# Kernel optimization log

Hardware: AMD Instinct MI355X
Metric: run time of the kernel (lower is better)

## Reference

```python
import jax, jax.numpy as jnp
import numpy as np

N_NODES = 100000  # static number of output segments for SpMM


def setup_inputs() -> dict:
    key = jax.random.key(0)
    k_x, k_r, k_c, k_v, k_w, k_b = jax.random.split(key, 6)
    N, E, F_IN, F_OUT = N_NODES, 1600000, 256, 128
    return {
        "input_features": jax.random.normal(k_x, (N, F_IN), dtype=jnp.float32),
        "edge_rows": jax.random.randint(k_r, (E,), 0, N, dtype=jnp.int32),
        "edge_cols": jax.random.randint(k_c, (E,), 0, N, dtype=jnp.int32),
        "edge_vals": jax.random.uniform(k_v, (E,), dtype=jnp.float32),
        "W": jax.random.normal(k_w, (F_OUT, F_IN), dtype=jnp.float32) * 0.02,
        "b": jax.random.normal(k_b, (F_OUT,), dtype=jnp.float32) * 0.02,
    }


def reference(input_features, edge_rows, edge_cols, edge_vals, W, b):
    # transformed = Linear(x) = x @ W^T + b   -> [N, F_OUT]
    transformed = jnp.einsum("nf,of->no", input_features, W) + b
    # SpMM: out[r] = sum_{edges e with row r} val[e] * transformed[col[e]]
    gathered = transformed[edge_cols] * edge_vals[:, None]  # [E, F_OUT]
    out = jax.ops.segment_sum(gathered, edge_rows, num_segments=N_NODES)
    return out
```

## Files before the change

kernel.cpp:

```cpp
#include <hip/hip_runtime.h>

#define N_NODES 100000
#define F_IN 256
#define F_OUT 128
#define NB 1563
#define SUBCAP 256

typedef __attribute__((ext_vector_type(8))) short bf16x8;
typedef __attribute__((ext_vector_type(4))) float f32x4;

__device__ inline unsigned short f2bf(float f) {
  unsigned u = __builtin_bit_cast(unsigned, f);
  u += 0x7fffu + ((u >> 16) & 1u);
  return (unsigned short)(u >> 16);
}

__device__ inline int xcd_id() {
  return __builtin_amdgcn_s_getreg((3 << 11) | (0 << 6) | 20) & 7;
}

__global__ __launch_bounds__(256) void gemm_kernel(
    const float* __restrict__ x, const float* __restrict__ W,
    const float* __restrict__ b, unsigned short* __restrict__ tout) {
  __shared__ unsigned short As[128][72];
  __shared__ unsigned short Bs[128][72];
  const int tid = threadIdx.x;
  const int wave = tid >> 6, lane = tid & 63;
  const int quad = lane >> 4, l16 = lane & 15;
  const int mw = (wave >> 1) * 64, nw = (wave & 1) * 64;
  const int blockM = blockIdx.x * 128;

  f32x4 acc[4][4];
#pragma unroll
  for (int i = 0; i < 4; ++i)
#pragma unroll
    for (int j = 0; j < 4; ++j) acc[i][j] = (f32x4){0.f, 0.f, 0.f, 0.f};

  const int row_s = tid >> 4;
  const int c4 = tid & 15;

  for (int kb = 0; kb < F_IN; kb += 64) {
#pragma unroll
    for (int i = 0; i < 8; ++i) {
      int r = row_s + i * 16;
      int node = blockM + r;
      float4 v = make_float4(0.f, 0.f, 0.f, 0.f);
      if (node < N_NODES) v = *(const float4*)(x + (size_t)node * F_IN + kb + c4 * 4);
      unsigned short* p = &As[r][c4 * 4];
      p[0] = f2bf(v.x); p[1] = f2bf(v.y); p[2] = f2bf(v.z); p[3] = f2bf(v.w);
    }
#pragma unroll
    for (int i = 0; i < 8; ++i) {
      int r = row_s + i * 16;
      float4 v = *(const float4*)(W + (size_t)r * F_IN + kb + c4 * 4);
      unsigned short* p = &Bs[r][c4 * 4];
      p[0] = f2bf(v.x); p[1] = f2bf(v.y); p[2] = f2bf(v.z); p[3] = f2bf(v.w);
    }
    __syncthreads();
#pragma unroll
    for (int ks = 0; ks < 2; ++ks) {
      bf16x8 a[4], bb[4];
#pragma unroll
      for (int t = 0; t < 4; ++t)
        a[t] = *(const bf16x8*)&As[mw + t * 16 + l16][ks * 32 + quad * 8];
#pragma unroll
      for (int t = 0; t < 4; ++t)
        bb[t] = *(const bf16x8*)&Bs[nw + t * 16 + l16][ks * 32 + quad * 8];
#pragma unroll
      for (int i = 0; i < 4; ++i)
#pragma unroll
        for (int j = 0; j < 4; ++j)
          acc[i][j] = __builtin_amdgcn_mfma_f32_16x16x32_bf16(a[i], bb[j], acc[i][j], 0, 0, 0);
    }
    __syncthreads();
  }
#pragma unroll
  for (int i = 0; i < 4; ++i) {
#pragma unroll
    for (int j = 0; j < 4; ++j) {
      int o = nw + j * 16 + l16;
      float bias = b[o];
#pragma unroll
      for (int r = 0; r < 4; ++r) {
        int node = blockM + mw + i * 16 + quad * 4 + r;
        if (node < N_NODES)
          tout[(size_t)node * F_OUT + o] = f2bf(acc[i][j][r] + bias);
      }
    }
  }
}

__global__ void phaseA_kernel(const int* __restrict__ rows, const int* __restrict__ cols,
                              const float* __restrict__ vals, int* __restrict__ cursor,
                              int2* __restrict__ staging, int E) {
  int i = blockIdx.x * blockDim.x + threadIdx.x;
  int xc = xcd_id();
  if (i < E) {
    int r = rows[i];
    int bkt = r >> 6;
    int p = atomicAdd(&cursor[(bkt * 8 + xc) * 16], 1);
    if (p < SUBCAP)
      staging[((size_t)bkt * 8 + xc) * SUBCAP + p] =
          make_int2(((r & 63) << 17) | cols[i], __float_as_int(vals[i]));
  }
}

__global__ __launch_bounds__(1024) void scan_buckets_kernel(
    const int* __restrict__ cursor, int* __restrict__ bucketOff) {
  __shared__ int s[1024];
  __shared__ int carry;
  if (threadIdx.x == 0) carry = 0;
  __syncthreads();
  for (int chunk = 0; chunk < NB; chunk += 1024) {
    int i = chunk + threadIdx.x;
    int v = 0;
    if (i < NB) {
#pragma unroll
      for (int s8 = 0; s8 < 8; ++s8) v += min(cursor[(i * 8 + s8) * 16], SUBCAP);
    }
    s[threadIdx.x] = v;
    __syncthreads();
    for (int off = 1; off < 1024; off <<= 1) {
      int t = (threadIdx.x >= off) ? s[threadIdx.x - off] : 0;
      __syncthreads();
      s[threadIdx.x] += t;
      __syncthreads();
    }
    if (i < NB) bucketOff[i] = carry + s[threadIdx.x] - v;
    __syncthreads();
    if (threadIdx.x == 1023) carry += s[1023];
    __syncthreads();
  }
}

__global__ __launch_bounds__(256) void phaseB_kernel(
    const int2* __restrict__ staging, const int* __restrict__ cursor,
    const int* __restrict__ bucketOff, int2* __restrict__ edata,
    int* __restrict__ rowOff, int* __restrict__ rowCnt) {
  int b = blockIdx.x;
  int base = bucketOff[b];
  __shared__ int rc[64];
  __shared__ int ro[64];
  __shared__ int scnt[8];
  if (threadIdx.x < 8) scnt[threadIdx.x] = min(cursor[(b * 8 + threadIdx.x) * 16], SUBCAP);
  if (threadIdx.x < 64) rc[threadIdx.x] = 0;
  __syncthreads();
#pragma unroll
  for (int s = 0; s < 8; ++s) {
    int cs = scnt[s];
    const int2* sp = staging + ((size_t)b * 8 + s) * SUBCAP;
    for (int i = threadIdx.x; i < cs; i += 256)
      atomicAdd(&rc[sp[i].x >> 17], 1);
  }
  __syncthreads();
  if (threadIdx.x < 64) {
    int v = rc[threadIdx.x];
    int sum = v;
#pragma unroll
    for (int off = 1; off < 64; off <<= 1) {
      int t = __shfl_up(sum, off, 64);
      if ((threadIdx.x & 63) >= off) sum += t;
    }
    ro[threadIdx.x] = sum - v;
    rc[threadIdx.x] = 0;
    int row = b * 64 + threadIdx.x;
    if (row < N_NODES) {
      rowOff[row] = base + sum - v;
      rowCnt[row] = v;
    }
  }
  __syncthreads();
#pragma unroll
  for (int s = 0; s < 8; ++s) {
    int cs = scnt[s];
    const int2* sp = staging + ((size_t)b * 8 + s) * SUBCAP;
    for (int i = threadIdx.x; i < cs; i += 256) {
      int2 e = sp[i];
      int rl = e.x >> 17;
      int slot = atomicAdd(&rc[rl], 1);
      edata[base + ro[rl] + slot] = make_int2(e.x & 0x1FFFF, e.y);
    }
  }
}

__global__ __launch_bounds__(256) void spmm_kernel(
    const unsigned short* __restrict__ tb, const int2* __restrict__ edata,
    const int* __restrict__ rowOff, const int* __restrict__ rowCnt,
    float* __restrict__ out) {
  int wave = (blockIdx.x * 256 + threadIdx.x) >> 6;
  int lane = threadIdx.x & 63;
  if (wave >= N_NODES) return;
  int start = rowOff[wave];
  int n = rowCnt[wave];
  float2 acc = make_float2(0.f, 0.f);
  for (int base = 0; base < n; base += 64) {
    int m = n - base;
    if (m > 64) m = 64;
    int c = 0;
    float v = 0.f;
    if (lane < m) {
      int2 e = edata[start + base + lane];
      c = e.x;
      v = __builtin_bit_cast(float, e.y);
    }
    for (int j0 = 0; j0 < m; j0 += 8) {
      unsigned t[8];
      float vj[8];
#pragma unroll
      for (int jj = 0; jj < 8; ++jj) {
        int cj = __shfl(c, j0 + jj, 64);
        vj[jj] = __shfl(v, j0 + jj, 64);
        t[jj] = *(const unsigned*)(tb + (size_t)cj * F_OUT + lane * 2);
      }
#pragma unroll
      for (int jj = 0; jj < 8; ++jj) {
        acc.x = fmaf(vj[jj], __builtin_bit_cast(float, t[jj] << 16), acc.x);
        acc.y = fmaf(vj[jj], __builtin_bit_cast(float, t[jj] & 0xffff0000u), acc.y);
      }
    }
  }
  ((float2*)out)[(size_t)wave * 64 + lane] = acc;
}

extern "C" void kernel_launch(void* const* d_in, const int* in_sizes, int n_in,
                              void* d_out, int out_size, void* d_ws, size_t ws_size,
                              hipStream_t stream) {
  const float* x    = (const float*)d_in[0];
  const int*   rows = (const int*)d_in[1];
  const int*   cols = (const int*)d_in[2];
  const float* vals = (const float*)d_in[3];
  const float* W    = (const float*)d_in[4];
  const float* b    = (const float*)d_in[5];
  float* out = (float*)d_out;
  const int E = in_sizes[1];

  const size_t region0 = (size_t)NB * 8 * SUBCAP * sizeof(int2);
  unsigned short* tb = (unsigned short*)d_ws;
  int2* staging  = (int2*)d_ws;
  int2* edata    = (int2*)((char*)d_ws + region0);
  int* cursor    = (int*)(edata + E);
  int* bucketOff = cursor + NB * 8 * 16;
  int* rowOff    = bucketOff + ((NB + 1) & ~1);
  int* rowCnt    = rowOff + N_NODES;

  hipMemsetAsync(cursor, 0, (size_t)NB * 8 * 16 * sizeof(int), stream);

  phaseA_kernel<<<(E + 255) / 256, 256, 0, stream>>>(rows, cols, vals, cursor, staging, E);
  scan_buckets_kernel<<<1, 1024, 0, stream>>>(cursor, bucketOff);
  phaseB_kernel<<<NB, 256, 0, stream>>>(staging, cursor, bucketOff, edata, rowOff, rowCnt);
  gemm_kernel<<<(N_NODES + 127) / 128, 256, 0, stream>>>(x, W, b, tb);
  spmm_kernel<<<(N_NODES + 3) / 4, 256, 0, stream>>>(tb, edata, rowOff, rowCnt, out);
}
```

Baseline: 366.8 us.

## Replace bucket scan with atomic allocation, prefetch GEMM tiles, preconvert W to bf16

Drops the single-block scan kernel. Each phaseB block now reserves its edge output range with an atomic add on a global counter, so buckets no longer land in row order in edata. W is converted to bf16 once inside extra phaseA blocks, and the GEMM loads it as 16-byte vectors. The GEMM also register-prefetches the next K-slice of x and W while the current slice's MFMAs run. This removes one serial kernel launch and overlaps global loads with compute, at the cost of more registers and non-deterministic edge placement.

Result: faster. 348.5 us (-5.0%).

```diff
diff --git a/kernel.cpp b/kernel.cpp
--- a/kernel.cpp
+++ b/kernel.cpp
@@ -20,8 +20,8 @@
 }
 
 __global__ __launch_bounds__(256) void gemm_kernel(
-    const float* __restrict__ x, const float* __restrict__ W,
-    const float* __restrict__ b, unsigned short* __restrict__ tout) {
+    const float* __restrict__ x, const unsigned short* __restrict__ wbf,
+    const float* __restrict__ bias, unsigned short* __restrict__ tout) {
   __shared__ unsigned short As[128][72];
   __shared__ unsigned short Bs[128][72];
   const int tid = threadIdx.x;
@@ -38,25 +38,44 @@
 
   const int row_s = tid >> 4;
   const int c4 = tid & 15;
+  const int row_b = tid >> 3;
+  const int c8 = tid & 7;
+
+  float4 pa[8];
+  bf16x8 pb[4];
+#pragma unroll
+  for (int i = 0; i < 8; ++i) {
+    int node = blockM + row_s + i * 16;
+    pa[i] = make_float4(0.f, 0.f, 0.f, 0.f);
+    if (node < N_NODES) pa[i] = *(const float4*)(x + (size_t)node * F_IN + c4 * 4);
+  }
+#pragma unroll
+  for (int i = 0; i < 4; ++i)
+    pb[i] = *(const bf16x8*)(wbf + (row_b + i * 32) * F_IN + c8 * 8);
 
   for (int kb = 0; kb < F_IN; kb += 64) {
 #pragma unroll
     for (int i = 0; i < 8; ++i) {
-      int r = row_s + i * 16;
-      int node = blockM + r;
-      float4 v = make_float4(0.f, 0.f, 0.f, 0.f);
-      if (node < N_NODES) v = *(const float4*)(x + (size_t)node * F_IN + kb + c4 * 4);
-      unsigned short* p = &As[r][c4 * 4];
-      p[0] = f2bf(v.x); p[1] = f2bf(v.y); p[2] = f2bf(v.z); p[3] = f2bf(v.w);
-    }
-#pragma unroll
-    for (int i = 0; i < 8; ++i) {
-      int r = row_s + i * 16;
-      float4 v = *(const float4*)(W + (size_t)r * F_IN + kb + c4 * 4);
-      unsigned short* p = &Bs[r][c4 * 4];
-      p[0] = f2bf(v.x); p[1] = f2bf(v.y); p[2] = f2bf(v.z); p[3] = f2bf(v.w);
-    }
+      unsigned short* p = &As[row_s + i * 16][c4 * 4];
+      p[0] = f2bf(pa[i].x); p[1] = f2bf(pa[i].y);
+      p[2] = f2bf(pa[i].z); p[3] = f2bf(pa[i].w);
+    }
+#pragma unroll
+    for (int i = 0; i < 4; ++i)
+      *(bf16x8*)&Bs[row_b + i * 32][c8 * 8] = pb[i];
     __syncthreads();
+    if (kb + 64 < F_IN) {
+      const int kn = kb + 64;
+#pragma unroll
+      for (int i = 0; i < 8; ++i) {
+        int node = blockM + row_s + i * 16;
+        if (node < N_NODES)
+          pa[i] = *(const float4*)(x + (size_t)node * F_IN + kn + c4 * 4);
+      }
+#pragma unroll
+      for (int i = 0; i < 4; ++i)
+        pb[i] = *(const bf16x8*)(wbf + (row_b + i * 32) * F_IN + kn + c8 * 8);
+    }
 #pragma unroll
     for (int ks = 0; ks < 2; ++ks) {
       bf16x8 a[4], bb[4];
@@ -79,12 +98,12 @@
 #pragma unroll
     for (int j = 0; j < 4; ++j) {
       int o = nw + j * 16 + l16;
-      float bias = b[o];
+      float bv = bias[o];
 #pragma unroll
       for (int r = 0; r < 4; ++r) {
         int node = blockM + mw + i * 16 + quad * 4 + r;
         if (node < N_NODES)
-          tout[(size_t)node * F_OUT + o] = f2bf(acc[i][j][r] + bias);
+          tout[(size_t)node * F_OUT + o] = f2bf(acc[i][j][r] + bv);
       }
     }
   }
@@ -92,7 +111,15 @@
 
 __global__ void phaseA_kernel(const int* __restrict__ rows, const int* __restrict__ cols,
                               const float* __restrict__ vals, int* __restrict__ cursor,
-                              int2* __restrict__ staging, int E) {
+                              int2* __restrict__ staging, int E, int edgeBlocks,
+                              const float* __restrict__ W, unsigned short* __restrict__ wbf) {
+  if (blockIdx.x >= edgeBlocks) {
+    int t = (blockIdx.x - edgeBlocks) * 256 + threadIdx.x;
+    float4 v = *(const float4*)(W + (size_t)t * 4);
+    unsigned short* p = wbf + (size_t)t * 4;
+    p[0] = f2bf(v.x); p[1] = f2bf(v.y); p[2] = f2bf(v.z); p[3] = f2bf(v.w);
+    return;
+  }
   int i = blockIdx.x * blockDim.x + threadIdx.x;
   int xc = xcd_id();
   if (i < E) {
@@ -105,43 +132,15 @@
   }
 }
 
-__global__ __launch_bounds__(1024) void scan_buckets_kernel(
-    const int* __restrict__ cursor, int* __restrict__ bucketOff) {
-  __shared__ int s[1024];
-  __shared__ int carry;
-  if (threadIdx.x == 0) carry = 0;
-  __syncthreads();
-  for (int chunk = 0; chunk < NB; chunk += 1024) {
-    int i = chunk + threadIdx.x;
-    int v = 0;
-    if (i < NB) {
-#pragma unroll
-      for (int s8 = 0; s8 < 8; ++s8) v += min(cursor[(i * 8 + s8) * 16], SUBCAP);
-    }
-    s[threadIdx.x] = v;
-    __syncthreads();
-    for (int off = 1; off < 1024; off <<= 1) {
-      int t = (threadIdx.x >= off) ? s[threadIdx.x - off] : 0;
-      __syncthreads();
-      s[threadIdx.x] += t;
-      __syncthreads();
-    }
-    if (i < NB) bucketOff[i] = carry + s[threadIdx.x] - v;
-    __syncthreads();
-    if (threadIdx.x == 1023) carry += s[1023];
-    __syncthreads();
-  }
-}
-
 __global__ __launch_bounds__(256) void phaseB_kernel(
     const int2* __restrict__ staging, const int* __restrict__ cursor,
-    const int* __restrict__ bucketOff, int2* __restrict__ edata,
+    int* __restrict__ allocCtr, int2* __restrict__ edata,
     int* __restrict__ rowOff, int* __restrict__ rowCnt) {
   int b = blockIdx.x;
-  int base = bucketOff[b];
   __shared__ int rc[64];
   __shared__ int ro[64];
   __shared__ int scnt[8];
+  __shared__ int base_s;
   if (threadIdx.x < 8) scnt[threadIdx.x] = min(cursor[(b * 8 + threadIdx.x) * 16], SUBCAP);
   if (threadIdx.x < 64) rc[threadIdx.x] = 0;
   __syncthreads();
@@ -153,23 +152,28 @@
       atomicAdd(&rc[sp[i].x >> 17], 1);
   }
   __syncthreads();
+  int v = 0;
   if (threadIdx.x < 64) {
-    int v = rc[threadIdx.x];
+    v = rc[threadIdx.x];
     int sum = v;
 #pragma unroll
     for (int off = 1; off < 64; off <<= 1) {
       int t = __shfl_up(sum, off, 64);
-      if ((threadIdx.x & 63) >= off) sum += t;
+      if (threadIdx.x >= off) sum += t;
     }
     ro[threadIdx.x] = sum - v;
     rc[threadIdx.x] = 0;
+    if (threadIdx.x == 63) base_s = atomicAdd(allocCtr, sum);
+  }
+  __syncthreads();
+  int base = base_s;
+  if (threadIdx.x < 64) {
     int row = b * 64 + threadIdx.x;
     if (row < N_NODES) {
-      rowOff[row] = base + sum - v;
+      rowOff[row] = base + ro[threadIdx.x];
       rowCnt[row] = v;
     }
   }
-  __syncthreads();
 #pragma unroll
   for (int s = 0; s < 8; ++s) {
     int cs = scnt[s];
@@ -239,15 +243,17 @@
   int2* staging  = (int2*)d_ws;
   int2* edata    = (int2*)((char*)d_ws + region0);
   int* cursor    = (int*)(edata + E);
-  int* bucketOff = cursor + NB * 8 * 16;
-  int* rowOff    = bucketOff + ((NB + 1) & ~1);
+  int* allocCtr  = cursor + NB * 8 * 16;
+  int* rowOff    = allocCtr + 16;
   int* rowCnt    = rowOff + N_NODES;
-
-  hipMemsetAsync(cursor, 0, (size_t)NB * 8 * 16 * sizeof(int), stream);
-
-  phaseA_kernel<<<(E + 255) / 256, 256, 0, stream>>>(rows, cols, vals, cursor, staging, E);
-  scan_buckets_kernel<<<1, 1024, 0, stream>>>(cursor, bucketOff);
-  phaseB_kernel<<<NB, 256, 0, stream>>>(staging, cursor, bucketOff, edata, rowOff, rowCnt);
-  gemm_kernel<<<(N_NODES + 127) / 128, 256, 0, stream>>>(x, W, b, tb);
+  unsigned short* wbf = (unsigned short*)(rowCnt + N_NODES);
+
+  hipMemsetAsync(cursor, 0, ((size_t)NB * 8 * 16 + 16) * sizeof(int), stream);
+
+  const int edgeBlocks = (E + 255) / 256;
+  phaseA_kernel<<<edgeBlocks + 32, 256, 0, stream>>>(rows, cols, vals, cursor, staging,
+                                                     E, edgeBlocks, W, wbf);
+  phaseB_kernel<<<NB, 256, 0, stream>>>(staging, cursor, allocCtr, edata, rowOff, rowCnt);
+  gemm_kernel<<<(N_NODES + 127) / 128, 256, 0, stream>>>(x, wbf, b, tb);
   spmm_kernel<<<(N_NODES + 3) / 4, 256, 0, stream>>>(tb, edata, rowOff, rowCnt, out);
 }
```
